# Kernel tuning notes

Hardware: AMD Instinct MI355X
Metric: run time of the kernel (lower is better)

Reference implementation:

```python
import jax, jax.numpy as jnp
import numpy as np

B, H, W, C = 8, 224, 224, 96
WS, SHIFT, HEADS = 7, 3, 3
N = WS * WS
HEAD_DIM = C // HEADS
SCALE = HEAD_DIM ** -0.5
EPS = 1e-5


def _build_shift_mask():
    # standard Swin shifted-window attention mask, values in {0, -100}
    img = np.zeros((H, W), np.float32)
    cnt = 0
    for hs in (slice(0, -WS), slice(-WS, -SHIFT), slice(-SHIFT, None)):
        for ws_ in (slice(0, -WS), slice(-WS, -SHIFT), slice(-SHIFT, None)):
            img[hs, ws_] = cnt
            cnt += 1
    mw = img.reshape(H // WS, WS, W // WS, WS).transpose(0, 2, 1, 3).reshape(-1, N)  # (nW, N)
    am = mw[:, None, :] - mw[:, :, None]
    am = np.where(am != 0, -100.0, 0.0).astype(np.float32)  # (nW, N, N)
    return np.tile(am, (B, 1, 1))  # (B*nW, N, N)


def setup_inputs() -> dict:
    key = jax.random.key(0)
    ks = jax.random.split(key, 6)
    s = 0.02
    return {
        "x": jax.random.normal(ks[0], (B, H, W, C), jnp.float32),
        "mask": jnp.asarray(_build_shift_mask()),
        "norm1_g": jnp.ones((C,), jnp.float32),
        "norm1_b": jnp.zeros((C,), jnp.float32),
        "qkv_w": jax.random.normal(ks[1], (3 * C, C), jnp.float32) * s,
        "qkv_b": jnp.zeros((3 * C,), jnp.float32),
        "proj_w": jax.random.normal(ks[2], (C, C), jnp.float32) * s,
        "proj_b": jnp.zeros((C,), jnp.float32),
        "norm2_g": jnp.ones((C,), jnp.float32),
        "norm2_b": jnp.zeros((C,), jnp.float32),
        "fc1_w": jax.random.normal(ks[3], (4 * C, C), jnp.float32) * s,
        "fc1_b": jnp.zeros((4 * C,), jnp.float32),
        "fc2_w": jax.random.normal(ks[4], (C, 4 * C), jnp.float32) * s,
        "fc2_b": jnp.zeros((C,), jnp.float32),
    }


def _ln(x, g, b):
    mu = jnp.mean(x, axis=-1, keepdims=True)
    var = jnp.mean(jnp.square(x - mu), axis=-1, keepdims=True)
    return (x - mu) * jax.lax.rsqrt(var + EPS) * g + b


def reference(x, mask, norm1_g, norm1_b, qkv_w, qkv_b, proj_w, proj_b,
              norm2_g, norm2_b, fc1_w, fc1_b, fc2_w, fc2_b):
    b, h, w, c = x.shape
    shortcut = x.reshape(b, h * w, c)
    xn = _ln(x, norm1_g, norm1_b)
    # cyclic shift
    xs = jnp.roll(xn, (-SHIFT, -SHIFT), axis=(1, 2))
    # window partition -> (B*nW, N, C)
    xw = xs.reshape(b, h // WS, WS, w // WS, WS, c).transpose(0, 1, 3, 2, 4, 5).reshape(-1, N, c)
    # window attention
    qkv = xw @ qkv_w.T + qkv_b                                  # (B_, N, 3C)
    qkv = qkv.reshape(-1, N, 3, HEADS, HEAD_DIM).transpose(2, 0, 3, 1, 4)
    q, k, v = qkv[0] * SCALE, qkv[1], qkv[2]                    # (B_, h, N, d)
    attn = jnp.einsum('bhnd,bhmd->bhnm', q, k) + mask[:, None]  # (B_, h, N, N)
    attn = jax.nn.softmax(attn, axis=-1)
    o = jnp.einsum('bhnm,bhmd->bhnd', attn, v).transpose(0, 2, 1, 3).reshape(-1, N, c)
    o = o @ proj_w.T + proj_b
    # window reverse
    o = o.reshape(b, h // WS, w // WS, WS, WS, c).transpose(0, 1, 3, 2, 4, 5).reshape(b, h, w, c)
    o = jnp.roll(o, (SHIFT, SHIFT), axis=(1, 2)).reshape(b, h * w, c)
    x = shortcut + o
    # MLP with exact (erf) GELU, as torch nn.GELU default
    y = _ln(x, norm2_g, norm2_b)
    y = jax.nn.gelu(y @ fc1_w.T + fc1_b, approximate=False)
    return x + (y @ fc2_w.T + fc2_b)
```

## Files before the change

### kernel.cpp

```cpp
#include <hip/hip_runtime.h>

typedef __attribute__((ext_vector_type(8))) short short8;
typedef __attribute__((ext_vector_type(4))) float floatx4;

#define MFMA(a,b,c) __builtin_amdgcn_mfma_f32_16x16x32_bf16(a,b,c,0,0,0)

__device__ __forceinline__ ushort f2bf(float f){ union{float f;uint i;}x; x.f=f; return (ushort)((x.i + 0x7fffu + ((x.i>>16)&1u))>>16); }
__device__ __forceinline__ short8 lds8(const ushort* p){ return *(const short8*)p; }

__global__ void convw_kernel(const float* __restrict__ qkvw,
                             const float* __restrict__ projw,
                             const float* __restrict__ f1w,
                             const float* __restrict__ f2w,
                             ushort* __restrict__ wb)
{
  int i = blockIdx.x*256 + threadIdx.x;
  float v;
  if      (i < 27648)  v = qkvw[i];
  else if (i < 36864)  v = projw[i-27648];
  else if (i < 73728)  v = f1w[i-36864];
  else if (i < 110592) v = f2w[i-73728];
  else return;
  wb[i] = f2bf(v);
}

__global__ __launch_bounds__(256) void swin_block_kernel(
    const float* __restrict__ x,
    const float* __restrict__ g1, const float* __restrict__ b1v,
    const ushort* __restrict__ qkv_wb, const float* __restrict__ qkv_b,
    const ushort* __restrict__ proj_wb, const float* __restrict__ proj_b,
    const float* __restrict__ g2, const float* __restrict__ b2v,
    const ushort* __restrict__ fc1_wb, const float* __restrict__ fc1_b,
    const ushort* __restrict__ fc2_wb, const float* __restrict__ fc2_b,
    float* __restrict__ out)
{
  __shared__ __align__(16) ushort sm[32000];
  __shared__ int sid[64];
  ushort* xn  = sm;
  ushort* Qb  = sm + 6656;
  ushort* Kb  = sm + 12800;
  ushort* Vt  = sm + 20480;
  ushort* Pb  = sm + 27392;
  float*  xrb = (float*)(sm + 6656);
  ushort* hb  = sm + 18944;

  const int tid  = threadIdx.x;
  const int w    = blockIdx.x;
  const int b    = w >> 10;
  const int wh   = (w >> 5) & 31;
  const int wwn  = w & 31;
  const int lane = tid & 63;
  const int wv   = tid >> 6;
  const int quad = lane >> 4;
  const int ln   = lane & 15;

  {
    const int n = tid >> 2, q = tid & 3;
    if (n < 49) {
      const int i = n / 7, j = n - 7*i;
      int hh = wh*7 + i + 3; if (hh >= 224) hh -= 224;
      int w2 = wwn*7 + j + 3; if (w2 >= 224) w2 -= 224;
      if (q == 0) {
        const int rr = (wh < 31) ? 0 : ((i < 4) ? 1 : 2);
        const int cr = (wwn < 31) ? 0 : ((j < 4) ? 1 : 2);
        sid[n] = rr*3 + cr;
      }
      const float* px = x + (((size_t)b*224 + hh)*224 + w2)*96 + q*24;
      float v[24]; float s = 0.f, s2 = 0.f;
      const float4* p4 = (const float4*)px;
      #pragma unroll
      for (int t = 0; t < 6; ++t) { float4 u = p4[t];
        v[t*4+0]=u.x; v[t*4+1]=u.y; v[t*4+2]=u.z; v[t*4+3]=u.w; }
      #pragma unroll
      for (int c = 0; c < 24; ++c) { s += v[c]; s2 += v[c]*v[c]; }
      s  += __shfl_xor(s, 1);  s  += __shfl_xor(s, 2);
      s2 += __shfl_xor(s2, 1); s2 += __shfl_xor(s2, 2);
      const float mu = s * (1.f/96.f);
      const float rs = rsqrtf(s2*(1.f/96.f) - mu*mu + 1e-5f);
      ushort* row = xn + n*104 + q*24;
      #pragma unroll
      for (int c = 0; c < 24; ++c)
        row[c] = f2bf((v[c]-mu)*rs*g1[q*24+c] + b1v[q*24+c]);
    }
    for (int idx = tid; idx < 15*104; idx += 256) xn[49*104 + idx] = 0;
  }
  __syncthreads();

  {
    const ushort* arow = xn + (wv*16 + ln)*104 + quad*8;
    short8 a0 = lds8(arow), a1 = lds8(arow+32), a2 = lds8(arow+64);
    for (int nt = 0; nt < 18; ++nt) {
      const ushort* wrow = qkv_wb + (nt*16 + ln)*96 + quad*8;
      floatx4 acc = {0.f,0.f,0.f,0.f};
      acc = MFMA(a0, lds8(wrow),    acc);
      acc = MFMA(a1, lds8(wrow+32), acc);
      acc = MFMA(a2, lds8(wrow+64), acc);
      const int col = nt*16 + ln;
      const float bias = qkv_b[col];
      const int ty = col / 96, hcol = col % 96, h = hcol >> 5, d = hcol & 31;
      #pragma unroll
      for (int reg = 0; reg < 4; ++reg) {
        const int r = wv*16 + quad*4 + reg;
        float val = acc[reg] + bias;
        if (ty == 0)      Qb[h*2048 + r*32 + d] = f2bf(val * 0.17677669529663689f);
        else if (ty == 1) Kb[h*2560 + r*40 + d] = f2bf(val);
        else              Vt[h*2304 + d*72 + r] = f2bf(val);
      }
    }
  }
  __syncthreads();

  int idrv[4], idcv[4];
  #pragma unroll
  for (int reg = 0; reg < 4; ++reg) {
    const int r = wv*16 + quad*4 + reg;
    idrv[reg] = (r < 49) ? sid[r] : -1;
  }
  #pragma unroll
  for (int nt = 0; nt < 4; ++nt) {
    const int c = nt*16 + ln;
    idcv[nt] = (c < 49) ? sid[c] : -2;
  }

  ushort* ob = xn;
  for (int h = 0; h < 3; ++h) {
    short8 aq = lds8(Qb + h*2048 + (wv*16 + ln)*32 + quad*8);
    floatx4 sc[4];
    #pragma unroll
    for (int nt = 0; nt < 4; ++nt) {
      short8 kb = lds8(Kb + h*2560 + (nt*16 + ln)*40 + quad*8);
      floatx4 z = {0.f,0.f,0.f,0.f};
      sc[nt] = MFMA(aq, kb, z);
    }
    #pragma unroll
    for (int reg = 0; reg < 4; ++reg) {
      float t[4]; float mx = -1e30f;
      #pragma unroll
      for (int nt = 0; nt < 4; ++nt) {
        float tv = -1e30f;
        if (idrv[reg] >= 0 && idcv[nt] >= 0)
          tv = sc[nt][reg] + ((idrv[reg] == idcv[nt]) ? 0.f : -100.f);
        t[nt] = tv; mx = fmaxf(mx, tv);
      }
      mx = fmaxf(mx, __shfl_xor(mx, 1));
      mx = fmaxf(mx, __shfl_xor(mx, 2));
      mx = fmaxf(mx, __shfl_xor(mx, 4));
      mx = fmaxf(mx, __shfl_xor(mx, 8));
      float e[4], sum = 0.f;
      #pragma unroll
      for (int nt = 0; nt < 4; ++nt) {
        e[nt] = (t[nt] > -1e29f) ? __expf(t[nt] - mx) : 0.f;
        sum += e[nt];
      }
      sum += __shfl_xor(sum, 1);
      sum += __shfl_xor(sum, 2);
      sum += __shfl_xor(sum, 4);
      sum += __shfl_xor(sum, 8);
      const float inv = (sum > 0.f) ? 1.f/sum : 0.f;
      #pragma unroll
      for (int nt = 0; nt < 4; ++nt)
        Pb[(wv*16 + quad*4 + reg)*72 + nt*16 + ln] = f2bf(e[nt]*inv);
    }
    __syncthreads();
    short8 p0 = lds8(Pb + (wv*16 + ln)*72 + quad*8);
    short8 p1 = lds8(Pb + (wv*16 + ln)*72 + 32 + quad*8);
    #pragma unroll
    for (int ntd = 0; ntd < 2; ++ntd) {
      floatx4 accO = {0.f,0.f,0.f,0.f};
      accO = MFMA(p0, lds8(Vt + h*2304 + (ntd*16+ln)*72 + quad*8),      accO);
      accO = MFMA(p1, lds8(Vt + h*2304 + (ntd*16+ln)*72 + 32 + quad*8), accO);
      #pragma unroll
      for (int reg = 0; reg < 4; ++reg)
        ob[(wv*16 + quad*4 + reg)*104 + h*32 + ntd*16 + ln] = f2bf(accO[reg]);
    }
    __syncthreads();
  }

  {
    const ushort* arow = ob + (wv*16 + ln)*104 + quad*8;
    short8 a0 = lds8(arow), a1 = lds8(arow+32), a2 = lds8(arow+64);
    for (int nt = 0; nt < 6; ++nt) {
      const ushort* wrow = proj_wb + (nt*16 + ln)*96 + quad*8;
      floatx4 acc = {0.f,0.f,0.f,0.f};
      acc = MFMA(a0, lds8(wrow),    acc);
      acc = MFMA(a1, lds8(wrow+32), acc);
      acc = MFMA(a2, lds8(wrow+64), acc);
      const int col = nt*16 + ln;
      const float bias = proj_b[col];
      #pragma unroll
      for (int reg = 0; reg < 4; ++reg) {
        const int r = wv*16 + quad*4 + reg;
        if (r < 49) {
          const int i = r / 7, j = r - 7*i;
          int hh = wh*7 + i + 3; if (hh >= 224) hh -= 224;
          int w2 = wwn*7 + j + 3; if (w2 >= 224) w2 -= 224;
          const size_t pos = (((size_t)b*224 + hh)*224 + w2)*96 + col;
          xrb[r*96 + col] = x[pos] + acc[reg] + bias;
        }
      }
    }
    for (int idx = tid; idx < 15*96; idx += 256) xrb[49*96 + idx] = 0.f;
  }
  __syncthreads();

  {
    const int n = tid >> 2, q = tid & 3;
    const float4* p4 = (const float4*)(xrb + n*96 + q*24);
    float v[24]; float s = 0.f, s2 = 0.f;
    #pragma unroll
    for (int t = 0; t < 6; ++t) { float4 u = p4[t];
      v[t*4+0]=u.x; v[t*4+1]=u.y; v[t*4+2]=u.z; v[t*4+3]=u.w; }
    #pragma unroll
    for (int c = 0; c < 24; ++c) { s += v[c]; s2 += v[c]*v[c]; }
    s  += __shfl_xor(s, 1);  s  += __shfl_xor(s, 2);
    s2 += __shfl_xor(s2, 1); s2 += __shfl_xor(s2, 2);
    const float mu = s * (1.f/96.f);
    const float rs = rsqrtf(s2*(1.f/96.f) - mu*mu + 1e-5f);
    ushort* row = xn + n*104 + q*24;
    #pragma unroll
    for (int c = 0; c < 24; ++c)
      row[c] = f2bf((v[c]-mu)*rs*g2[q*24+c] + b2v[q*24+c]);
  }
  __syncthreads();

  const int rloc = (wv & 1) * 16;
  const int p    = wv >> 1;
  for (int half = 0; half < 2; ++half) {
    {
      const ushort* arow = xn + (half*32 + rloc + ln)*104 + quad*8;
      short8 a0 = lds8(arow), a1 = lds8(arow+32), a2 = lds8(arow+64);
      for (int t = 0; t < 12; ++t) {
        const int nt = p*12 + t;
        const ushort* wrow = fc1_wb + (nt*16 + ln)*96 + quad*8;
        floatx4 acc = {0.f,0.f,0.f,0.f};
        acc = MFMA(a0, lds8(wrow),    acc);
        acc = MFMA(a1, lds8(wrow+32), acc);
        acc = MFMA(a2, lds8(wrow+64), acc);
        const int col = nt*16 + ln;
        const float bias = fc1_b[col];
        #pragma unroll
        for (int reg = 0; reg < 4; ++reg) {
          const float vv = acc[reg] + bias;
          hb[(rloc + quad*4 + reg)*392 + col] =
              f2bf(0.5f*vv*(1.f + erff(vv*0.70710678118654752f)));
        }
      }
    }
    __syncthreads();
    {
      short8 ap[12];
      const ushort* prow = hb + (rloc + ln)*392 + quad*8;
      #pragma unroll
      for (int kt = 0; kt < 12; ++kt) ap[kt] = lds8(prow + kt*32);
      for (int t = 0; t < 3; ++t) {
        const int nt = p*3 + t;
        const ushort* wrow = fc2_wb + (nt*16 + ln)*384 + quad*8;
        floatx4 acc = {0.f,0.f,0.f,0.f};
        #pragma unroll
        for (int kt = 0; kt < 12; ++kt) acc = MFMA(ap[kt], lds8(wrow + kt*32), acc);
        const int col = nt*16 + ln;
        const float bias = fc2_b[col];
        #pragma unroll
        for (int reg = 0; reg < 4; ++reg) {
          const int r = half*32 + rloc + quad*4 + reg;
          if (r < 49) {
            const int i = r / 7, j = r - 7*i;
            int hh = wh*7 + i + 3; if (hh >= 224) hh -= 224;
            int w2 = wwn*7 + j + 3; if (w2 >= 224) w2 -= 224;
            const size_t pos = (((size_t)b*224 + hh)*224 + w2)*96 + col;
            out[pos] = xrb[r*96 + col] + acc[reg] + bias;
          }
        }
      }
    }
    __syncthreads();
  }
}

extern "C" void kernel_launch(void* const* d_in, const int* in_sizes, int n_in,
                              void* d_out, int out_size, void* d_ws, size_t ws_size,
                              hipStream_t stream) {
  int ix=-1, iq=-1, ip=-1, if1=-1, if2=-1, largest=0;
  for (int i = 0; i < n_in; ++i) {
    const int s = in_sizes[i];
    if (s == 38535168 && ix < 0) ix = i;
    else if (s == 27648 && iq < 0) iq = i;
    else if (s == 9216 && ip < 0) ip = i;
    else if (s == 36864) { if (if1 < 0) if1 = i; else if (if2 < 0) if2 = i; }
    if (in_sizes[i] >= in_sizes[largest]) largest = i;
  }
  if (ix < 0) ix = largest;
  if (iq < 0) iq = 4;
  if (ip < 0) ip = 6;
  if (if1 < 0) if1 = 10;
  if (if2 < 0) if2 = 12;

  const float* x    = (const float*)d_in[ix];
  const float* n1g  = (const float*)d_in[2];
  const float* n1b  = (const float*)d_in[3];
  const float* qkvw = (const float*)d_in[iq];
  const float* qkvb = (const float*)d_in[5];
  const float* pw   = (const float*)d_in[ip];
  const float* pb   = (const float*)d_in[7];
  const float* n2g  = (const float*)d_in[8];
  const float* n2b  = (const float*)d_in[9];
  const float* f1w  = (const float*)d_in[if1];
  const float* f1b  = (const float*)d_in[11];
  const float* f2w  = (const float*)d_in[if2];
  const float* f2b  = (const float*)d_in[13];
  float* outp = (float*)d_out;
  ushort* wb = (ushort*)d_ws;

  convw_kernel<<<432, 256, 0, stream>>>(qkvw, pw, f1w, f2w, wb);
  swin_block_kernel<<<8192, 256, 0, stream>>>(
      x, n1g, n1b, wb, qkvb, wb + 27648, pb,
      n2g, n2b, wb + 36864, f1b, wb + 73728, f2b, outp);
}
```

Before: 940.0 us.

## Shrink LDS footprint via per-head QKV and global residual to raise occupancy

Moves the QKV projection inside the head loop, so only one head's Q, K and V^T sit in shared memory at a time. The MLP hidden buffer now aliases the residual buffer, and the post-attention residual is written to the output in global memory and then accumulated with `+=`. Together these cut the static LDS allocation from about 64 KB to about 38 KB, and `__launch_bounds__(256,4)` asks for four blocks per CU to hide latency. In exchange the kernel gets extra barriers per head and an extra global write and read of the output tensor, which may hit L2.

```diff
diff --git a/kernel.cpp b/kernel.cpp
--- a/kernel.cpp
+++ b/kernel.cpp
@@ -24,7 +24,7 @@
   wb[i] = f2bf(v);
 }
 
-__global__ __launch_bounds__(256) void swin_block_kernel(
+__global__ __launch_bounds__(256,4) void swin_block_kernel(
     const float* __restrict__ x,
     const float* __restrict__ g1, const float* __restrict__ b1v,
     const ushort* __restrict__ qkv_wb, const float* __restrict__ qkv_b,
@@ -34,15 +34,15 @@
     const ushort* __restrict__ fc2_wb, const float* __restrict__ fc2_b,
     float* __restrict__ out)
 {
-  __shared__ __align__(16) ushort sm[32000];
+  __shared__ __align__(16) ushort sm[19200];
   __shared__ int sid[64];
   ushort* xn  = sm;
-  ushort* Qb  = sm + 6656;
-  ushort* Kb  = sm + 12800;
-  ushort* Vt  = sm + 20480;
-  ushort* Pb  = sm + 27392;
+  ushort* Qh  = sm + 6656;
+  ushort* Kh  = sm + 8704;
+  ushort* Vh  = sm + 11264;
+  ushort* Pb  = sm + 13568;
   float*  xrb = (float*)(sm + 6656);
-  ushort* hb  = sm + 18944;
+  ushort* hb  = sm + 6656;
 
   const int tid  = threadIdx.x;
   const int w    = blockIdx.x;
@@ -86,30 +86,11 @@
   }
   __syncthreads();
 
+  short8 a0, a1, a2;
   {
     const ushort* arow = xn + (wv*16 + ln)*104 + quad*8;
-    short8 a0 = lds8(arow), a1 = lds8(arow+32), a2 = lds8(arow+64);
-    for (int nt = 0; nt < 18; ++nt) {
-      const ushort* wrow = qkv_wb + (nt*16 + ln)*96 + quad*8;
-      floatx4 acc = {0.f,0.f,0.f,0.f};
-      acc = MFMA(a0, lds8(wrow),    acc);
-      acc = MFMA(a1, lds8(wrow+32), acc);
-      acc = MFMA(a2, lds8(wrow+64), acc);
-      const int col = nt*16 + ln;
-      const float bias = qkv_b[col];
-      const int ty = col / 96, hcol = col % 96, h = hcol >> 5, d = hcol & 31;
-      #pragma unroll
-      for (int reg = 0; reg < 4; ++reg) {
-        const int r = wv*16 + quad*4 + reg;
-        float val = acc[reg] + bias;
-        if (ty == 0)      Qb[h*2048 + r*32 + d] = f2bf(val * 0.17677669529663689f);
-        else if (ty == 1) Kb[h*2560 + r*40 + d] = f2bf(val);
-        else              Vt[h*2304 + d*72 + r] = f2bf(val);
-      }
-    }
-  }
-  __syncthreads();
-
+    a0 = lds8(arow); a1 = lds8(arow+32); a2 = lds8(arow+64);
+  }
   int idrv[4], idcv[4];
   #pragma unroll
   for (int reg = 0; reg < 4; ++reg) {
@@ -124,67 +105,94 @@
 
   ushort* ob = xn;
   for (int h = 0; h < 3; ++h) {
-    short8 aq = lds8(Qb + h*2048 + (wv*16 + ln)*32 + quad*8);
-    floatx4 sc[4];
     #pragma unroll
-    for (int nt = 0; nt < 4; ++nt) {
-      short8 kb = lds8(Kb + h*2560 + (nt*16 + ln)*40 + quad*8);
-      floatx4 z = {0.f,0.f,0.f,0.f};
-      sc[nt] = MFMA(aq, kb, z);
-    }
-    #pragma unroll
-    for (int reg = 0; reg < 4; ++reg) {
-      float t[4]; float mx = -1e30f;
-      #pragma unroll
-      for (int nt = 0; nt < 4; ++nt) {
-        float tv = -1e30f;
-        if (idrv[reg] >= 0 && idcv[nt] >= 0)
-          tv = sc[nt][reg] + ((idrv[reg] == idcv[nt]) ? 0.f : -100.f);
-        t[nt] = tv; mx = fmaxf(mx, tv);
-      }
-      mx = fmaxf(mx, __shfl_xor(mx, 1));
-      mx = fmaxf(mx, __shfl_xor(mx, 2));
-      mx = fmaxf(mx, __shfl_xor(mx, 4));
-      mx = fmaxf(mx, __shfl_xor(mx, 8));
-      float e[4], sum = 0.f;
-      #pragma unroll
-      for (int nt = 0; nt < 4; ++nt) {
-        e[nt] = (t[nt] > -1e29f) ? __expf(t[nt] - mx) : 0.f;
-        sum += e[nt];
-      }
-      sum += __shfl_xor(sum, 1);
-      sum += __shfl_xor(sum, 2);
-      sum += __shfl_xor(sum, 4);
-      sum += __shfl_xor(sum, 8);
-      const float inv = (sum > 0.f) ? 1.f/sum : 0.f;
-      #pragma unroll
-      for (int nt = 0; nt < 4; ++nt)
-        Pb[(wv*16 + quad*4 + reg)*72 + nt*16 + ln] = f2bf(e[nt]*inv);
-    }
-    __syncthreads();
-    short8 p0 = lds8(Pb + (wv*16 + ln)*72 + quad*8);
-    short8 p1 = lds8(Pb + (wv*16 + ln)*72 + 32 + quad*8);
-    #pragma unroll
-    for (int ntd = 0; ntd < 2; ++ntd) {
-      floatx4 accO = {0.f,0.f,0.f,0.f};
-      accO = MFMA(p0, lds8(Vt + h*2304 + (ntd*16+ln)*72 + quad*8),      accO);
-      accO = MFMA(p1, lds8(Vt + h*2304 + (ntd*16+ln)*72 + 32 + quad*8), accO);
-      #pragma unroll
-      for (int reg = 0; reg < 4; ++reg)
-        ob[(wv*16 + quad*4 + reg)*104 + h*32 + ntd*16 + ln] = f2bf(accO[reg]);
-    }
-    __syncthreads();
-  }
-
-  {
-    const ushort* arow = ob + (wv*16 + ln)*104 + quad*8;
-    short8 a0 = lds8(arow), a1 = lds8(arow+32), a2 = lds8(arow+64);
     for (int nt = 0; nt < 6; ++nt) {
-      const ushort* wrow = proj_wb + (nt*16 + ln)*96 + quad*8;
+      const int sec = nt >> 1, sub = nt & 1;
+      const int colw = sec*96 + h*32 + sub*16 + ln;
+      const ushort* wrow = qkv_wb + colw*96 + quad*8;
       floatx4 acc = {0.f,0.f,0.f,0.f};
       acc = MFMA(a0, lds8(wrow),    acc);
       acc = MFMA(a1, lds8(wrow+32), acc);
       acc = MFMA(a2, lds8(wrow+64), acc);
+      const float bias = qkv_b[colw];
+      const int d = sub*16 + ln;
+      #pragma unroll
+      for (int reg = 0; reg < 4; ++reg) {
+        const int r = wv*16 + quad*4 + reg;
+        float val = acc[reg] + bias;
+        if (sec == 0)      Qh[r*32 + d] = f2bf(val * 0.17677669529663689f);
+        else if (sec == 1) Kh[r*40 + d] = f2bf(val);
+        else               Vh[d*72 + r] = f2bf(val);
+      }
+    }
+    __syncthreads();
+
+    {
+      short8 aq = lds8(Qh + (wv*16 + ln)*32 + quad*8);
+      floatx4 sc[4];
+      #pragma unroll
+      for (int nt = 0; nt < 4; ++nt) {
+        short8 kb = lds8(Kh + (nt*16 + ln)*40 + quad*8);
+        floatx4 z = {0.f,0.f,0.f,0.f};
+        sc[nt] = MFMA(aq, kb, z);
+      }
+      #pragma unroll
+      for (int reg = 0; reg < 4; ++reg) {
+        float t[4]; float mx = -1e30f;
+        #pragma unroll
+        for (int nt = 0; nt < 4; ++nt) {
+          float tv = -1e30f;
+          if (idrv[reg] >= 0 && idcv[nt] >= 0)
+            tv = sc[nt][reg] + ((idrv[reg] == idcv[nt]) ? 0.f : -100.f);
+          t[nt] = tv; mx = fmaxf(mx, tv);
+        }
+        mx = fmaxf(mx, __shfl_xor(mx, 1));
+        mx = fmaxf(mx, __shfl_xor(mx, 2));
+        mx = fmaxf(mx, __shfl_xor(mx, 4));
+        mx = fmaxf(mx, __shfl_xor(mx, 8));
+        float e[4], sum = 0.f;
+        #pragma unroll
+        for (int nt = 0; nt < 4; ++nt) {
+          e[nt] = (t[nt] > -1e29f) ? __expf(t[nt] - mx) : 0.f;
+          sum += e[nt];
+        }
+        sum += __shfl_xor(sum, 1);
+        sum += __shfl_xor(sum, 2);
+        sum += __shfl_xor(sum, 4);
+        sum += __shfl_xor(sum, 8);
+        const float inv = (sum > 0.f) ? 1.f/sum : 0.f;
+        #pragma unroll
+        for (int nt = 0; nt < 4; ++nt)
+          Pb[(wv*16 + quad*4 + reg)*72 + nt*16 + ln] = f2bf(e[nt]*inv);
+      }
+    }
+    __syncthreads();
+
+    {
+      short8 p0 = lds8(Pb + (wv*16 + ln)*72 + quad*8);
+      short8 p1 = lds8(Pb + (wv*16 + ln)*72 + 32 + quad*8);
+      #pragma unroll
+      for (int ntd = 0; ntd < 2; ++ntd) {
+        floatx4 accO = {0.f,0.f,0.f,0.f};
+        accO = MFMA(p0, lds8(Vh + (ntd*16+ln)*72 + quad*8),      accO);
+        accO = MFMA(p1, lds8(Vh + (ntd*16+ln)*72 + 32 + quad*8), accO);
+        #pragma unroll
+        for (int reg = 0; reg < 4; ++reg)
+          ob[(wv*16 + quad*4 + reg)*104 + h*32 + ntd*16 + ln] = f2bf(accO[reg]);
+      }
+    }
+    __syncthreads();
+  }
+
+  {
+    const ushort* arow = ob + (wv*16 + ln)*104 + quad*8;
+    short8 o0 = lds8(arow), o1 = lds8(arow+32), o2 = lds8(arow+64);
+    for (int nt = 0; nt < 6; ++nt) {
+      const ushort* wrow = proj_wb + (nt*16 + ln)*96 + quad*8;
+      floatx4 acc = {0.f,0.f,0.f,0.f};
+      acc = MFMA(o0, lds8(wrow),    acc);
+      acc = MFMA(o1, lds8(wrow+32), acc);
+      acc = MFMA(o2, lds8(wrow+64), acc);
       const int col = nt*16 + ln;
       const float bias = proj_b[col];
       #pragma unroll
@@ -195,7 +203,9 @@
           int hh = wh*7 + i + 3; if (hh >= 224) hh -= 224;
           int w2 = wwn*7 + j + 3; if (w2 >= 224) w2 -= 224;
           const size_t pos = (((size_t)b*224 + hh)*224 + w2)*96 + col;
-          xrb[r*96 + col] = x[pos] + acc[reg] + bias;
+          const float val = x[pos] + acc[reg] + bias;
+          xrb[r*96 + col] = val;
+          out[pos] = val;
         }
       }
     }
@@ -228,14 +238,14 @@
   for (int half = 0; half < 2; ++half) {
     {
       const ushort* arow = xn + (half*32 + rloc + ln)*104 + quad*8;
-      short8 a0 = lds8(arow), a1 = lds8(arow+32), a2 = lds8(arow+64);
+      short8 m0 = lds8(arow), m1 = lds8(arow+32), m2 = lds8(arow+64);
       for (int t = 0; t < 12; ++t) {
         const int nt = p*12 + t;
         const ushort* wrow = fc1_wb + (nt*16 + ln)*96 + quad*8;
         floatx4 acc = {0.f,0.f,0.f,0.f};
-        acc = MFMA(a0, lds8(wrow),    acc);
-        acc = MFMA(a1, lds8(wrow+32), acc);
-        acc = MFMA(a2, lds8(wrow+64), acc);
+        acc = MFMA(m0, lds8(wrow),    acc);
+        acc = MFMA(m1, lds8(wrow+32), acc);
+        acc = MFMA(m2, lds8(wrow+64), acc);
         const int col = nt*16 + ln;
         const float bias = fc1_b[col];
         #pragma unroll
@@ -268,7 +278,7 @@
             int hh = wh*7 + i + 3; if (hh >= 224) hh -= 224;
             int w2 = wwn*7 + j + 3; if (w2 >= 224) w2 -= 224;
             const size_t pos = (((size_t)b*224 + hh)*224 + w2)*96 + col;
-            out[pos] = xrb[r*96 + col] + acc[reg] + bias;
+            out[pos] += acc[reg] + bias;
           }
         }
       }
```

Result: no change. 927.3 us (-1.3%).
